# Optimization experiments

Measured on AMD Instinct MI355X. Metric: run time of the kernel, lower is better.

## Reference

```python
import jax, jax.numpy as jnp
import numpy as np

HID = 768
HEADS = 12
HEAD_LEN = HID // HEADS
SCALE_INV = 1.0 / np.sqrt(HEAD_LEN).astype(np.float32)


def setup_inputs() -> dict:
    key = jax.random.key(0)
    ks = jax.random.split(key, 5)
    std = 1.0 / np.sqrt(HID)
    return {
        "x": jax.random.normal(ks[0], (1, 4096, HID), dtype=jnp.float32),
        "w_q": jax.random.normal(ks[1], (HID, HID), dtype=jnp.float32) * std,
        "w_k": jax.random.normal(ks[2], (HID, HID), dtype=jnp.float32) * std,
        "w_v": jax.random.normal(ks[3], (HID, HID), dtype=jnp.float32) * std,
        "w_fc": jax.random.normal(ks[4], (HID, HID), dtype=jnp.float32) * std,
    }


def reference(x, w_q, w_k, w_v, w_fc):
    B, S, D = x.shape
    # torch Linear weight layout [out, in]: y = x @ W.T
    def proj_heads(w):
        y = jnp.einsum("bsd,ed->bse", x, w)
        return y.reshape(B, S, HEADS, HEAD_LEN).transpose(0, 2, 1, 3)  # bhsd
    q = proj_heads(w_q)
    k = proj_heads(w_k)
    v = proj_heads(w_v)
    scores = SCALE_INV * jnp.einsum("bhqd,bhkd->bhqk", q, k)
    attn = jax.nn.softmax(scores, axis=-1)
    out = jnp.einsum("bhqk,bhkd->bhqd", attn, v)
    out = out.transpose(0, 2, 1, 3).reshape(B, S, D)
    return jnp.einsum("bsd,ed->bse", out, w_fc)
```

## Files before the change

kernel.cpp:

```cpp
#include <hip/hip_runtime.h>
#include <hip/hip_bf16.h>

#define S_LEN 4096
#define HID 768
#define NHEAD 12
#define HL 64
#define PSS 72

typedef __attribute__((ext_vector_type(8))) short short8;
typedef __attribute__((ext_vector_type(4))) float f32x4;
using bf16 = __hip_bfloat16;

__device__ __forceinline__ void gl2lds16(const void* g, void* l) {
  __builtin_amdgcn_global_load_lds((__attribute__((address_space(1))) void*)(g),
                                   (__attribute__((address_space(3))) void*)(l),
                                   16, 0, 0);
}

__device__ __forceinline__ f32x4 mfma_bf16(short8 a, short8 b, f32x4 c) {
  return __builtin_amdgcn_mfma_f32_16x16x32_bf16(a, b, c, 0, 0, 0);
}

__device__ __forceinline__ void storeC(float* C, long idx, float v) { C[idx] = v; }
__device__ __forceinline__ void storeC(bf16* C, long idx, float v) { C[idx] = __float2bfloat16(v); }

#define BAR() asm volatile("s_waitcnt lgkmcnt(0)\n\ts_barrier" ::: "memory")

__global__ __launch_bounds__(256) void cvt_all(
    const float* __restrict__ x, const float* __restrict__ wq,
    const float* __restrict__ wk, const float* __restrict__ wv,
    const float* __restrict__ wfc, bf16* __restrict__ xb, bf16* __restrict__ wqb,
    bf16* __restrict__ wkb, bf16* __restrict__ wvb, bf16* __restrict__ wfcb) {
  const long NX = (long)S_LEN * HID;
  const long NW = (long)HID * HID;
  long i = ((long)blockIdx.x * 256 + threadIdx.x) * 4;
  const float* src;
  bf16* dst;
  long off;
  if (i < NX) {
    src = x; dst = xb; off = i;
  } else {
    long j = i - NX;
    int wsel = (int)(j / NW);
    off = j - (long)wsel * NW;
    src = wsel == 0 ? wq : wsel == 1 ? wk : wsel == 2 ? wv : wfc;
    dst = wsel == 0 ? wqb : wsel == 1 ? wkb : wsel == 2 ? wvb : wfcb;
  }
  float4 v = *(const float4*)(src + off);
  bf16 h0 = __float2bfloat16(v.x), h1 = __float2bfloat16(v.y);
  bf16 h2 = __float2bfloat16(v.z), h3 = __float2bfloat16(v.w);
  ushort4 o;
  o.x = *(unsigned short*)&h0; o.y = *(unsigned short*)&h1;
  o.z = *(unsigned short*)&h2; o.w = *(unsigned short*)&h3;
  *(ushort4*)(dst + off) = o;
}

template <typename OT>
__global__ __launch_bounds__(256) void gemm_bt(
    const bf16* __restrict__ A, const bf16* __restrict__ B0,
    const bf16* __restrict__ B1, const bf16* __restrict__ B2,
    OT* __restrict__ C0, OT* __restrict__ C1, OT* __restrict__ C2, float qscale) {
  constexpr int K = HID;
  __shared__ __align__(16) bf16 As[128 * 32];
  __shared__ __align__(16) bf16 Bs[128 * 32];
  const int z = blockIdx.z;
  const bf16* B = (z == 0) ? B0 : (z == 1) ? B1 : B2;
  OT* C = (z == 0) ? C0 : (z == 1) ? C1 : C2;
  const float sc = (z == 0) ? qscale : 1.0f;
  const int bm = blockIdx.y, bn = blockIdx.x;
  const int t = threadIdx.x, lane = t & 63, w = t >> 6;
  const int wm = w >> 1, wn = w & 1;
  const int q4 = lane >> 4, c16 = lane & 15;
  const int srow = lane >> 2, scol = (lane & 3) * 8;
  const bf16* Ab = A + (long)bm * 128 * K;
  const bf16* Bb = B + (long)bn * 128 * K;
  f32x4 acc[4][4] = {};
  for (int k0 = 0; k0 < K; k0 += 32) {
#pragma unroll
    for (int r = 0; r < 2; ++r) {
      int rowb = r * 64 + w * 16;
      gl2lds16(Ab + (long)(rowb + srow) * K + k0 + scol, &As[rowb * 32]);
      gl2lds16(Bb + (long)(rowb + srow) * K + k0 + scol, &Bs[rowb * 32]);
    }
    __syncthreads();
    short8 af[4], bfv[4];
#pragma unroll
    for (int i = 0; i < 4; ++i)
      af[i] = *(const short8*)&As[(wm * 64 + i * 16 + c16) * 32 + q4 * 8];
#pragma unroll
    for (int j = 0; j < 4; ++j)
      bfv[j] = *(const short8*)&Bs[(wn * 64 + j * 16 + c16) * 32 + q4 * 8];
#pragma unroll
    for (int i = 0; i < 4; ++i)
#pragma unroll
      for (int j = 0; j < 4; ++j)
        acc[i][j] = mfma_bf16(af[i], bfv[j], acc[i][j]);
    __syncthreads();
  }
  const long crow0 = (long)bm * 128 + wm * 64;
  const int ccol0 = bn * 128 + wn * 64;
#pragma unroll
  for (int i = 0; i < 4; ++i)
#pragma unroll
    for (int j = 0; j < 4; ++j)
#pragma unroll
      for (int r = 0; r < 4; ++r) {
        long row = crow0 + i * 16 + q4 * 4 + r;
        int col = ccol0 + j * 16 + c16;
        storeC(C, row * HID + col, sc * acc[i][j][r]);
      }
}

__global__ __launch_bounds__(256) void gemm_fc(const bf16* __restrict__ A,
                                               const bf16* __restrict__ B,
                                               float* __restrict__ C) {
  __shared__ __align__(16) bf16 As[128 * 32];
  __shared__ __align__(16) bf16 Bs[64 * 32];
  const int bm = blockIdx.y, bn = blockIdx.x;
  const int t = threadIdx.x, lane = t & 63, w = t >> 6;
  const int q4 = lane >> 4, c16 = lane & 15;
  const int srow = lane >> 2, scol = (lane & 3) * 8;
  const bf16* Ab = A + (long)bm * 128 * HID;
  const bf16* Bb = B + (long)bn * 64 * HID;
  f32x4 acc[2][4] = {};
  for (int k0 = 0; k0 < HID; k0 += 32) {
#pragma unroll
    for (int r = 0; r < 2; ++r) {
      int rowb = w * 32 + r * 16;
      gl2lds16(Ab + (long)(rowb + srow) * HID + k0 + scol, &As[rowb * 32]);
    }
    gl2lds16(Bb + (long)(w * 16 + srow) * HID + k0 + scol, &Bs[w * 16 * 32]);
    __syncthreads();
    short8 af[2], bfv[4];
#pragma unroll
    for (int i = 0; i < 2; ++i)
      af[i] = *(const short8*)&As[(w * 32 + i * 16 + c16) * 32 + q4 * 8];
#pragma unroll
    for (int j = 0; j < 4; ++j)
      bfv[j] = *(const short8*)&Bs[(j * 16 + c16) * 32 + q4 * 8];
#pragma unroll
    for (int i = 0; i < 2; ++i)
#pragma unroll
      for (int j = 0; j < 4; ++j)
        acc[i][j] = mfma_bf16(af[i], bfv[j], acc[i][j]);
    __syncthreads();
  }
#pragma unroll
  for (int i = 0; i < 2; ++i)
#pragma unroll
    for (int j = 0; j < 4; ++j)
#pragma unroll
      for (int r = 0; r < 4; ++r) {
        long row = (long)bm * 128 + w * 32 + i * 16 + q4 * 4 + r;
        int col = bn * 64 + j * 16 + c16;
        C[row * HID + col] = acc[i][j][r];
      }
}

__global__ __launch_bounds__(256) void transpose_v(const bf16* __restrict__ V,
                                                   bf16* __restrict__ Vt) {
  __shared__ unsigned short tile[64][65];
  const int bs = blockIdx.x * 64;
  const int be = blockIdx.y * 64;
  const int t = threadIdx.x;
#pragma unroll
  for (int p = 0; p < 4; ++p) {
    int i = p * 256 + t;
    int r = i >> 4;
    int c = (i & 15) * 4;
    ushort4 v = *(const ushort4*)((const unsigned short*)V + (long)(bs + r) * HID + be + c);
    tile[r][c] = v.x; tile[r][c + 1] = v.y; tile[r][c + 2] = v.z; tile[r][c + 3] = v.w;
  }
  __syncthreads();
#pragma unroll
  for (int p = 0; p < 4; ++p) {
    int i = p * 256 + t;
    int r = i >> 4;
    int c = (i & 15) * 4;
    ushort4 v;
    v.x = tile[c][r]; v.y = tile[c + 1][r]; v.z = tile[c + 2][r]; v.w = tile[c + 3][r];
    *(ushort4*)((unsigned short*)Vt + (long)(be + r) * S_LEN + bs + c) = v;
  }
}

__global__ __launch_bounds__(256, 3) void flash_attn(const bf16* __restrict__ Q,
                                                     const bf16* __restrict__ Kg,
                                                     const bf16* __restrict__ Vt,
                                                     bf16* __restrict__ O) {
  __shared__ __align__(16) bf16 Ps[64 * PSS];
  __shared__ float Lred[4][64];
  const int qt = blockIdx.x, h = blockIdx.y;
  const int t = threadIdx.x, lane = t & 63, w = t >> 6;
  const int q4 = lane >> 4, c16 = lane & 15;
  const int s0 = qt * 64;

  short8 qf[2][4];
  {
    const bf16* Qb = Q + (long)(s0 + c16) * HID + h * HL + q4 * 8;
#pragma unroll
    for (int j = 0; j < 4; ++j)
#pragma unroll
      for (int ks = 0; ks < 2; ++ks)
        qf[ks][j] = *(const short8*)(Qb + (long)j * 16 * HID + ks * 32);
  }
  const bf16* kp = Kg + (long)(w * 16 + c16) * HID + h * HL + q4 * 8;
  const bf16* vp = Vt + (long)(h * HL + w * 16 + c16) * S_LEN + q4 * 8;

  float l_part[4] = {0.f, 0.f, 0.f, 0.f};
  f32x4 o_acc[4] = {};
  short8 kf0 = *(const short8*)(kp), kf1 = *(const short8*)(kp + 32);
  short8 vf0 = *(const short8*)(vp), vf1 = *(const short8*)(vp + 32);

  for (int kt = 0; kt < S_LEN / 64; ++kt) {
    f32x4 sacc[4] = {};
#pragma unroll
    for (int j = 0; j < 4; ++j) sacc[j] = mfma_bf16(kf0, qf[0][j], sacc[j]);
#pragma unroll
    for (int j = 0; j < 4; ++j) sacc[j] = mfma_bf16(kf1, qf[1][j], sacc[j]);

    const bf16* kpn = kp + 64 * HID;
    const bf16* vpn = vp + 64;
    if (kt == S_LEN / 64 - 1) { kpn = kp; vpn = vp; }
    short8 nk0 = *(const short8*)(kpn), nk1 = *(const short8*)(kpn + 32);
    short8 nv0 = *(const short8*)(vpn), nv1 = *(const short8*)(vpn + 32);

#pragma unroll
    for (int j = 0; j < 4; ++j) {
      float p0 = __builtin_amdgcn_exp2f(sacc[j][0]);
      float p1 = __builtin_amdgcn_exp2f(sacc[j][1]);
      float p2 = __builtin_amdgcn_exp2f(sacc[j][2]);
      float p3 = __builtin_amdgcn_exp2f(sacc[j][3]);
      l_part[j] += (p0 + p1) + (p2 + p3);
      bf16 b0 = __float2bfloat16(p0), b1 = __float2bfloat16(p1);
      bf16 b2 = __float2bfloat16(p2), b3 = __float2bfloat16(p3);
      short4 pk;
      pk.x = *(short*)&b0; pk.y = *(short*)&b1; pk.z = *(short*)&b2; pk.w = *(short*)&b3;
      *(short4*)&Ps[(j * 16 + c16) * PSS + w * 16 + q4 * 4] = pk;
    }
    BAR();

#pragma unroll
    for (int ks = 0; ks < 2; ++ks) {
      short8 vfk = ks ? vf1 : vf0;
#pragma unroll
      for (int j = 0; j < 4; ++j) {
        short8 pf = *(const short8*)&Ps[(j * 16 + c16) * PSS + ks * 32 + q4 * 8];
        o_acc[j] = mfma_bf16(vfk, pf, o_acc[j]);
      }
    }
    BAR();

    kf0 = nk0; kf1 = nk1; vf0 = nv0; vf1 = nv1;
    kp = kpn; vp = vpn;
  }

#pragma unroll
  for (int j = 0; j < 4; ++j) {
    float s = l_part[j];
    s += __shfl_xor(s, 16, 64);
    s += __shfl_xor(s, 32, 64);
    Lred[w][j * 16 + c16] = s;
  }
  BAR();
#pragma unroll
  for (int j = 0; j < 4; ++j) {
    int q = j * 16 + c16;
    float lt = Lred[0][q] + Lred[1][q] + Lred[2][q] + Lred[3][q];
    float rl = 1.0f / lt;
    float v0 = o_acc[j][0] * rl, v1 = o_acc[j][1] * rl;
    float v2 = o_acc[j][2] * rl, v3 = o_acc[j][3] * rl;
    bf16 b0 = __float2bfloat16(v0), b1 = __float2bfloat16(v1);
    bf16 b2 = __float2bfloat16(v2), b3 = __float2bfloat16(v3);
    short4 pk;
    pk.x = *(short*)&b0; pk.y = *(short*)&b1; pk.z = *(short*)&b2; pk.w = *(short*)&b3;
    *(short4*)&O[(long)(s0 + q) * HID + h * HL + w * 16 + q4 * 4] = pk;
  }
}

extern "C" void kernel_launch(void* const* d_in, const int* in_sizes, int n_in,
                              void* d_out, int out_size, void* d_ws, size_t ws_size,
                              hipStream_t stream) {
  const float* x = (const float*)d_in[0];
  const float* wq = (const float*)d_in[1];
  const float* wk = (const float*)d_in[2];
  const float* wv = (const float*)d_in[3];
  const float* wfc = (const float*)d_in[4];
  float* out = (float*)d_out;

  const long NBIG = (long)S_LEN * HID * sizeof(bf16);
  const long NWB = (long)HID * HID * sizeof(bf16);
  char* p = (char*)d_ws;
  bf16* xb = (bf16*)p;   p += NBIG;
  bf16* wqb = (bf16*)p;  p += NWB;
  bf16* wkb = (bf16*)p;  p += NWB;
  bf16* wvb = (bf16*)p;  p += NWB;
  bf16* wfcb = (bf16*)p; p += NWB;
  bf16* Qb = (bf16*)p;   p += NBIG;
  bf16* Kb = (bf16*)p;   p += NBIG;
  bf16* Vb = (bf16*)p;   p += NBIG;
  bf16* Vtb = (bf16*)p;  p += NBIG;
  bf16* Ob = (bf16*)p;   p += NBIG;

  const float c1 = 0.125f * 1.44269504088896340736f;

  const long total4 = ((long)S_LEN * HID + 4L * HID * HID) / 4;
  cvt_all<<<(int)(total4 / 256), 256, 0, stream>>>(x, wq, wk, wv, wfc, xb, wqb, wkb,
                                                   wvb, wfcb);
  gemm_bt<bf16><<<dim3(HID / 128, S_LEN / 128, 3), 256, 0, stream>>>(
      xb, wqb, wkb, wvb, Qb, Kb, Vb, c1);
  transpose_v<<<dim3(S_LEN / 64, HID / 64), 256, 0, stream>>>(Vb, Vtb);
  flash_attn<<<dim3(S_LEN / 64, NHEAD), 256, 0, stream>>>(Qb, Kb, Vtb, Ob);
  gemm_fc<<<dim3(HID / 64, S_LEN / 128), 256, 0, stream>>>(Ob, wfcb, out);
}
```

Measured before the change: 209.6 us.

## Split attention over two KV halves with combine kernel, double-buffer P tile

Flash attention now splits the key/value sequence into two halves along a new grid dimension, doubling block count from 768 to 1536 to better fill the GPU. Each half writes unnormalized fp32 partial outputs and row sums to scratch, and a new combine kernel merges them, normalizes and writes bf16. The P staging tile is double-buffered with an XOR swizzle instead of padding, which removes one barrier per iteration. V loads are moved after the PV MFMAs, and the workspace is reordered so the scratch reuses the space of buffers that are no longer needed. The cost is extra fp32 partial traffic and one more kernel launch.

```diff
diff --git a/kernel.cpp b/kernel.cpp
--- a/kernel.cpp
+++ b/kernel.cpp
@@ -5,7 +5,6 @@
 #define HID 768
 #define NHEAD 12
 #define HL 64
-#define PSS 72
 
 typedef __attribute__((ext_vector_type(8))) short short8;
 typedef __attribute__((ext_vector_type(4))) float f32x4;
@@ -183,16 +182,17 @@
   }
 }
 
-__global__ __launch_bounds__(256, 3) void flash_attn(const bf16* __restrict__ Q,
-                                                     const bf16* __restrict__ Kg,
-                                                     const bf16* __restrict__ Vt,
-                                                     bf16* __restrict__ O) {
-  __shared__ __align__(16) bf16 Ps[64 * PSS];
+__global__ __launch_bounds__(256, 5) void flash_attn(
+    const bf16* __restrict__ Q, const bf16* __restrict__ Kg,
+    const bf16* __restrict__ Vt, float* __restrict__ Opart,
+    float* __restrict__ Lpart) {
+  __shared__ __align__(16) bf16 Ps[2][64 * 64];
   __shared__ float Lred[4][64];
-  const int qt = blockIdx.x, h = blockIdx.y;
+  const int qt = blockIdx.x, h = blockIdx.y, sp = blockIdx.z;
   const int t = threadIdx.x, lane = t & 63, w = t >> 6;
   const int q4 = lane >> 4, c16 = lane & 15;
   const int s0 = qt * 64;
+  const int e7 = c16 & 7;
 
   short8 qf[2][4];
   {
@@ -203,26 +203,28 @@
       for (int ks = 0; ks < 2; ++ks)
         qf[ks][j] = *(const short8*)(Qb + (long)j * 16 * HID + ks * 32);
   }
-  const bf16* kp = Kg + (long)(w * 16 + c16) * HID + h * HL + q4 * 8;
-  const bf16* vp = Vt + (long)(h * HL + w * 16 + c16) * S_LEN + q4 * 8;
+  const bf16* kp = Kg + (long)(sp * 2048 + w * 16 + c16) * HID + h * HL + q4 * 8;
+  const bf16* vp = Vt + (long)(h * HL + w * 16 + c16) * S_LEN + sp * 2048 + q4 * 8;
 
   float l_part[4] = {0.f, 0.f, 0.f, 0.f};
   f32x4 o_acc[4] = {};
   short8 kf0 = *(const short8*)(kp), kf1 = *(const short8*)(kp + 32);
   short8 vf0 = *(const short8*)(vp), vf1 = *(const short8*)(vp + 32);
 
-  for (int kt = 0; kt < S_LEN / 64; ++kt) {
+  const int wr_off = ((w * 2 + (q4 >> 1)) ^ e7) * 8 + (q4 & 1) * 4;
+
+  for (int kt = 0; kt < 32; ++kt) {
+    bf16* Pb = Ps[kt & 1];
     f32x4 sacc[4] = {};
 #pragma unroll
     for (int j = 0; j < 4; ++j) sacc[j] = mfma_bf16(kf0, qf[0][j], sacc[j]);
 #pragma unroll
     for (int j = 0; j < 4; ++j) sacc[j] = mfma_bf16(kf1, qf[1][j], sacc[j]);
 
-    const bf16* kpn = kp + 64 * HID;
-    const bf16* vpn = vp + 64;
-    if (kt == S_LEN / 64 - 1) { kpn = kp; vpn = vp; }
-    short8 nk0 = *(const short8*)(kpn), nk1 = *(const short8*)(kpn + 32);
-    short8 nv0 = *(const short8*)(vpn), nv1 = *(const short8*)(vpn + 32);
+    const bf16* kpn = (kt == 31) ? kp : kp + 64 * HID;
+    kf0 = *(const short8*)(kpn);
+    kf1 = *(const short8*)(kpn + 32);
+    kp = kpn;
 
 #pragma unroll
     for (int j = 0; j < 4; ++j) {
@@ -235,7 +237,7 @@
       bf16 b2 = __float2bfloat16(p2), b3 = __float2bfloat16(p3);
       short4 pk;
       pk.x = *(short*)&b0; pk.y = *(short*)&b1; pk.z = *(short*)&b2; pk.w = *(short*)&b3;
-      *(short4*)&Ps[(j * 16 + c16) * PSS + w * 16 + q4 * 4] = pk;
+      *(short4*)&Pb[(j * 16 + c16) * 64 + wr_off] = pk;
     }
     BAR();
 
@@ -244,14 +246,14 @@
       short8 vfk = ks ? vf1 : vf0;
 #pragma unroll
       for (int j = 0; j < 4; ++j) {
-        short8 pf = *(const short8*)&Ps[(j * 16 + c16) * PSS + ks * 32 + q4 * 8];
+        short8 pf = *(const short8*)&Pb[(j * 16 + c16) * 64 + ((ks * 4 + q4) ^ e7) * 8];
         o_acc[j] = mfma_bf16(vfk, pf, o_acc[j]);
       }
     }
-    BAR();
-
-    kf0 = nk0; kf1 = nk1; vf0 = nv0; vf1 = nv1;
-    kp = kpn; vp = vpn;
+    const bf16* vpn = (kt == 31) ? vp : vp + 64;
+    vf0 = *(const short8*)(vpn);
+    vf1 = *(const short8*)(vpn + 32);
+    vp = vpn;
   }
 
 #pragma unroll
@@ -261,19 +263,46 @@
     s += __shfl_xor(s, 32, 64);
     Lred[w][j * 16 + c16] = s;
   }
-  BAR();
+  __syncthreads();
+  const long bb = (long)(sp * 64 + qt) * NHEAD + h;
 #pragma unroll
   for (int j = 0; j < 4; ++j) {
     int q = j * 16 + c16;
     float lt = Lred[0][q] + Lred[1][q] + Lred[2][q] + Lred[3][q];
-    float rl = 1.0f / lt;
-    float v0 = o_acc[j][0] * rl, v1 = o_acc[j][1] * rl;
-    float v2 = o_acc[j][2] * rl, v3 = o_acc[j][3] * rl;
-    bf16 b0 = __float2bfloat16(v0), b1 = __float2bfloat16(v1);
-    bf16 b2 = __float2bfloat16(v2), b3 = __float2bfloat16(v3);
-    short4 pk;
-    pk.x = *(short*)&b0; pk.y = *(short*)&b1; pk.z = *(short*)&b2; pk.w = *(short*)&b3;
-    *(short4*)&O[(long)(s0 + q) * HID + h * HL + w * 16 + q4 * 4] = pk;
+    if (w == 0) Lpart[bb * 64 + q] = lt;
+    float4 st;
+    st.x = o_acc[j][0]; st.y = o_acc[j][1]; st.z = o_acc[j][2]; st.w = o_acc[j][3];
+    *(float4*)&Opart[bb * 4096 + (long)q * 64 + w * 16 + q4 * 4] = st;
+  }
+}
+
+__global__ __launch_bounds__(256) void combine(const float* __restrict__ Opart,
+                                               const float* __restrict__ Lpart,
+                                               bf16* __restrict__ Ob) {
+  const int qt = blockIdx.x, h = blockIdx.y;
+  const long b0 = (long)qt * NHEAD + h;
+  const long b1 = (long)(64 + qt) * NHEAD + h;
+  const int t = threadIdx.x;
+  const int q = t >> 2, dc = (t & 3) * 16;
+  const float rl = 1.0f / (Lpart[b0 * 64 + q] + Lpart[b1 * 64 + q]);
+  const float* p0 = Opart + b0 * 4096 + (long)q * 64 + dc;
+  const float* p1 = Opart + b1 * 4096 + (long)q * 64 + dc;
+  bf16* ob = Ob + (long)(qt * 64 + q) * HID + h * HL + dc;
+#pragma unroll
+  for (int half = 0; half < 2; ++half) {
+    short8 pk;
+#pragma unroll
+    for (int i = 0; i < 2; ++i) {
+      float4 a = *(const float4*)(p0 + half * 8 + i * 4);
+      float4 b = *(const float4*)(p1 + half * 8 + i * 4);
+      float v0 = (a.x + b.x) * rl, v1 = (a.y + b.y) * rl;
+      float v2 = (a.z + b.z) * rl, v3 = (a.w + b.w) * rl;
+      bf16 h0 = __float2bfloat16(v0), h1 = __float2bfloat16(v1);
+      bf16 h2 = __float2bfloat16(v2), h3 = __float2bfloat16(v3);
+      pk[i * 4 + 0] = *(short*)&h0; pk[i * 4 + 1] = *(short*)&h1;
+      pk[i * 4 + 2] = *(short*)&h2; pk[i * 4 + 3] = *(short*)&h3;
+    }
+    *(short8*)(ob + half * 8) = pk;
   }
 }
 
@@ -290,16 +319,19 @@
   const long NBIG = (long)S_LEN * HID * sizeof(bf16);
   const long NWB = (long)HID * HID * sizeof(bf16);
   char* p = (char*)d_ws;
+  bf16* wfcb = (bf16*)p; p += NWB;
+  bf16* Qb = (bf16*)p;   p += NBIG;
+  bf16* Kb = (bf16*)p;   p += NBIG;
+  bf16* Vtb = (bf16*)p;  p += NBIG;
+  bf16* Ob = (bf16*)p;   p += NBIG;
+  char* scratch = p;
   bf16* xb = (bf16*)p;   p += NBIG;
   bf16* wqb = (bf16*)p;  p += NWB;
   bf16* wkb = (bf16*)p;  p += NWB;
   bf16* wvb = (bf16*)p;  p += NWB;
-  bf16* wfcb = (bf16*)p; p += NWB;
-  bf16* Qb = (bf16*)p;   p += NBIG;
-  bf16* Kb = (bf16*)p;   p += NBIG;
-  bf16* Vb = (bf16*)p;   p += NBIG;
-  bf16* Vtb = (bf16*)p;  p += NBIG;
-  bf16* Ob = (bf16*)p;   p += NBIG;
+  bf16* Vb = (bf16*)p;
+  float* Opart = (float*)scratch;
+  float* Lpart = (float*)(scratch + (long)2 * 64 * NHEAD * 4096 * sizeof(float));
 
   const float c1 = 0.125f * 1.44269504088896340736f;
 
@@ -309,6 +341,8 @@
   gemm_bt<bf16><<<dim3(HID / 128, S_LEN / 128, 3), 256, 0, stream>>>(
       xb, wqb, wkb, wvb, Qb, Kb, Vb, c1);
   transpose_v<<<dim3(S_LEN / 64, HID / 64), 256, 0, stream>>>(Vb, Vtb);
-  flash_attn<<<dim3(S_LEN / 64, NHEAD), 256, 0, stream>>>(Qb, Kb, Vtb, Ob);
+  flash_attn<<<dim3(S_LEN / 64, NHEAD, 2), 256, 0, stream>>>(Qb, Kb, Vtb, Opart,
+                                                             Lpart);
+  combine<<<dim3(S_LEN / 64, NHEAD), 256, 0, stream>>>(Opart, Lpart, Ob);
   gemm_fc<<<dim3(HID / 64, S_LEN / 128), 256, 0, stream>>>(Ob, wfcb, out);
 }
```

Measured after the change: 287.1 us. 37.0% more time.

## Process 128-key tiles with double-buffered swizzled P in LDS

Applied to the files above, without the earlier changes.

The flash attention loop now handles 128 keys per iteration instead of 64, so each wave computes two 16-row score chunks. The P tile moves to a double-buffered 128-wide LDS array with an XOR swizzle in place of padding, which removes the second barrier per iteration. Packing now uses paired bf16 conversion. This halves the barrier count and loop overhead, but raises register use (more K/V fragments and score accumulators) and LDS use, which may lower occupancy under launch_bounds(256,3).

```diff
diff --git a/kernel.cpp b/kernel.cpp
--- a/kernel.cpp
+++ b/kernel.cpp
@@ -5,7 +5,6 @@
 #define HID 768
 #define NHEAD 12
 #define HL 64
-#define PSS 72
 
 typedef __attribute__((ext_vector_type(8))) short short8;
 typedef __attribute__((ext_vector_type(4))) float f32x4;
@@ -187,7 +186,7 @@
                                                      const bf16* __restrict__ Kg,
                                                      const bf16* __restrict__ Vt,
                                                      bf16* __restrict__ O) {
-  __shared__ __align__(16) bf16 Ps[64 * PSS];
+  __shared__ __align__(16) bf16 Ps[2][64 * 128];
   __shared__ float Lred[4][64];
   const int qt = blockIdx.x, h = blockIdx.y;
   const int t = threadIdx.x, lane = t & 63, w = t >> 6;
@@ -203,55 +202,71 @@
       for (int ks = 0; ks < 2; ++ks)
         qf[ks][j] = *(const short8*)(Qb + (long)j * 16 * HID + ks * 32);
   }
-  const bf16* kp = Kg + (long)(w * 16 + c16) * HID + h * HL + q4 * 8;
+  const bf16* kp = Kg + (long)(w * 32 + c16) * HID + h * HL + q4 * 8;
   const bf16* vp = Vt + (long)(h * HL + w * 16 + c16) * S_LEN + q4 * 8;
 
   float l_part[4] = {0.f, 0.f, 0.f, 0.f};
   f32x4 o_acc[4] = {};
-  short8 kf0 = *(const short8*)(kp), kf1 = *(const short8*)(kp + 32);
-  short8 vf0 = *(const short8*)(vp), vf1 = *(const short8*)(vp + 32);
-
-  for (int kt = 0; kt < S_LEN / 64; ++kt) {
-    f32x4 sacc[4] = {};
-#pragma unroll
-    for (int j = 0; j < 4; ++j) sacc[j] = mfma_bf16(kf0, qf[0][j], sacc[j]);
-#pragma unroll
-    for (int j = 0; j < 4; ++j) sacc[j] = mfma_bf16(kf1, qf[1][j], sacc[j]);
-
-    const bf16* kpn = kp + 64 * HID;
-    const bf16* vpn = vp + 64;
-    if (kt == S_LEN / 64 - 1) { kpn = kp; vpn = vp; }
-    short8 nk0 = *(const short8*)(kpn), nk1 = *(const short8*)(kpn + 32);
-    short8 nv0 = *(const short8*)(vpn), nv1 = *(const short8*)(vpn + 32);
-
-#pragma unroll
-    for (int j = 0; j < 4; ++j) {
-      float p0 = __builtin_amdgcn_exp2f(sacc[j][0]);
-      float p1 = __builtin_amdgcn_exp2f(sacc[j][1]);
-      float p2 = __builtin_amdgcn_exp2f(sacc[j][2]);
-      float p3 = __builtin_amdgcn_exp2f(sacc[j][3]);
-      l_part[j] += (p0 + p1) + (p2 + p3);
-      bf16 b0 = __float2bfloat16(p0), b1 = __float2bfloat16(p1);
-      bf16 b2 = __float2bfloat16(p2), b3 = __float2bfloat16(p3);
-      short4 pk;
-      pk.x = *(short*)&b0; pk.y = *(short*)&b1; pk.z = *(short*)&b2; pk.w = *(short*)&b3;
-      *(short4*)&Ps[(j * 16 + c16) * PSS + w * 16 + q4 * 4] = pk;
-    }
-    BAR();
-
-#pragma unroll
-    for (int ks = 0; ks < 2; ++ks) {
-      short8 vfk = ks ? vf1 : vf0;
+  short8 kf[2][2], vf[4];
+#pragma unroll
+  for (int rr = 0; rr < 2; ++rr)
+#pragma unroll
+    for (int ks = 0; ks < 2; ++ks)
+      kf[rr][ks] = *(const short8*)(kp + (long)rr * 16 * HID + ks * 32);
+#pragma unroll
+  for (int kc = 0; kc < 4; ++kc) vf[kc] = *(const short8*)(vp + kc * 32);
+
+  for (int kt = 0; kt < S_LEN / 128; ++kt) {
+    bf16* Pb = Ps[kt & 1];
+    f32x4 sacc[2][4] = {};
+#pragma unroll
+    for (int rr = 0; rr < 2; ++rr)
+#pragma unroll
+      for (int ks = 0; ks < 2; ++ks)
+#pragma unroll
+        for (int j = 0; j < 4; ++j)
+          sacc[rr][j] = mfma_bf16(kf[rr][ks], qf[ks][j], sacc[rr][j]);
+
+    const bf16* kpn = (kt == S_LEN / 128 - 1) ? kp : kp + 128 * HID;
+#pragma unroll
+    for (int rr = 0; rr < 2; ++rr)
+#pragma unroll
+      for (int ks = 0; ks < 2; ++ks)
+        kf[rr][ks] = *(const short8*)(kpn + (long)rr * 16 * HID + ks * 32);
+    kp = kpn;
+
+#pragma unroll
+    for (int rr = 0; rr < 2; ++rr) {
+      const int wch = ((w * 4 + rr * 2 + (q4 >> 1)));
 #pragma unroll
       for (int j = 0; j < 4; ++j) {
-        short8 pf = *(const short8*)&Ps[(j * 16 + c16) * PSS + ks * 32 + q4 * 8];
-        o_acc[j] = mfma_bf16(vfk, pf, o_acc[j]);
+        float p0 = __builtin_amdgcn_exp2f(sacc[rr][j][0]);
+        float p1 = __builtin_amdgcn_exp2f(sacc[rr][j][1]);
+        float p2 = __builtin_amdgcn_exp2f(sacc[rr][j][2]);
+        float p3 = __builtin_amdgcn_exp2f(sacc[rr][j][3]);
+        l_part[j] += (p0 + p1) + (p2 + p3);
+        __hip_bfloat162 a01 = __float22bfloat162_rn(float2{p0, p1});
+        __hip_bfloat162 a23 = __float22bfloat162_rn(float2{p2, p3});
+        int2 pk;
+        pk.x = *(int*)&a01;
+        pk.y = *(int*)&a23;
+        *(int2*)&Pb[(j * 16 + c16) * 128 + (wch ^ c16) * 8 + (q4 & 1) * 4] = pk;
       }
     }
     BAR();
 
-    kf0 = nk0; kf1 = nk1; vf0 = nv0; vf1 = nv1;
-    kp = kpn; vp = vpn;
+#pragma unroll
+    for (int kc = 0; kc < 4; ++kc) {
+#pragma unroll
+      for (int j = 0; j < 4; ++j) {
+        short8 pf = *(const short8*)&Pb[(j * 16 + c16) * 128 + ((kc * 4 + q4) ^ c16) * 8];
+        o_acc[j] = mfma_bf16(vf[kc], pf, o_acc[j]);
+      }
+    }
+    const bf16* vpn = (kt == S_LEN / 128 - 1) ? vp : vp + 128;
+#pragma unroll
+    for (int kc = 0; kc < 4; ++kc) vf[kc] = *(const short8*)(vpn + kc * 32);
+    vp = vpn;
   }
 
 #pragma unroll
@@ -261,7 +276,7 @@
     s += __shfl_xor(s, 32, 64);
     Lred[w][j * 16 + c16] = s;
   }
-  BAR();
+  __syncthreads();
 #pragma unroll
   for (int j = 0; j < 4; ++j) {
     int q = j * 16 + c16;
```

After: 211.0 us. Within noise of the previous version (+0.7%).
